# Kernel tuning notes

Measured on AMD Instinct MI355X. Metric: run time of the kernel, lower is better.

Reference implementation:

```python
import jax, jax.numpy as jnp
import numpy as np

B, IN, OUT = 8192, 512, 1024

def setup_inputs() -> dict:
    key = jax.random.key(0)
    k1, k2 = jax.random.split(key)
    return {
        "input": jax.random.normal(k1, (B, IN), dtype=jnp.float32),
        "centres": jax.random.normal(k2, (OUT, IN), dtype=jnp.float32),
        "log_sigmas": jnp.zeros((OUT,), dtype=jnp.float32),
    }

def reference(input, centres, log_sigmas):
    x_sq = jnp.sum(input * input, axis=-1, keepdims=True)          # [B, 1]
    c_sq = jnp.sum(centres * centres, axis=-1)                     # [OUT]
    cross = input @ centres.T                                      # [B, OUT] GEMM
    d2 = jnp.maximum(x_sq - 2.0 * cross + c_sq[None, :], 0.0)
    distances = jnp.sqrt(d2) / jnp.exp(log_sigmas)[None, :]        # [B, OUT]
    # gaussian basis function: phi(alpha) = exp(-alpha^2)
    return jnp.exp(-(distances * distances))
```

## Files before the change

### kernel.cpp

```cpp
#include <hip/hip_runtime.h>
#include <hip/hip_bf16.h>


#define B_ROWS 8192
#define IN_K   512
#define OUT_N  1024

#define BM 128
#define BN 128
#define BK 32
#define LDT 40

typedef __attribute__((ext_vector_type(8))) __bf16 bf16x8;
typedef __attribute__((ext_vector_type(4))) __bf16 bf16x4;
typedef __attribute__((ext_vector_type(4))) float  floatx4;

__global__ void rowsumsq_512(const float* __restrict__ x, float* __restrict__ out, int rows) {
    int gt   = blockIdx.x * blockDim.x + threadIdx.x;
    int wave = gt >> 6;
    int lane = threadIdx.x & 63;
    if (wave >= rows) return;
    const float4* r4 = reinterpret_cast<const float4*>(x + (size_t)wave * IN_K);
    float4 a = r4[lane];
    float4 b = r4[lane + 64];
    float s = a.x*a.x + a.y*a.y + a.z*a.z + a.w*a.w
            + b.x*b.x + b.y*b.y + b.z*b.z + b.w*b.w;
    #pragma unroll
    for (int off = 32; off; off >>= 1) s += __shfl_xor(s, off, 64);
    if (lane == 0) out[wave] = s;
}

__global__ __launch_bounds__(256, 2) void rbf_gemm(
    const float* __restrict__ X,
    const float* __restrict__ C,
    const float* __restrict__ LS,
    const float* __restrict__ xsq,
    const float* __restrict__ csq,
    float* __restrict__ out)
{
    __shared__ __bf16 As[BM * LDT];
    __shared__ __bf16 Bs[BN * LDT];

    const int tid  = threadIdx.x;
    const int bn   = blockIdx.x & 7;
    const int bm   = blockIdx.x >> 3;
    const int brow = bm * BM;
    const int bcol = bn * BN;
    const int w    = tid >> 6;
    const int lane = tid & 63;
    const int wr   = w >> 1;
    const int wc   = w & 1;
    const int l15  = lane & 15;
    const int l4   = lane >> 4;

    floatx4 acc[4][4];
    #pragma unroll
    for (int m = 0; m < 4; ++m)
        #pragma unroll
        for (int n = 0; n < 4; ++n)
            acc[m][n] = (floatx4){0.f, 0.f, 0.f, 0.f};

    float4 ar[4], br[4];

    auto load_tile = [&](int kt, float4* a, float4* b) {
        #pragma unroll
        for (int i = 0; i < 4; ++i) {
            int lin = i * 256 + tid;
            int r   = lin >> 3;
            int c4  = lin & 7;
            a[i] = *reinterpret_cast<const float4*>(X + (size_t)(brow + r) * IN_K + kt * BK + c4 * 4);
            b[i] = *reinterpret_cast<const float4*>(C + (size_t)(bcol + r) * IN_K + kt * BK + c4 * 4);
        }
    };
    auto store_tile = [&](const float4* a, const float4* b) {
        #pragma unroll
        for (int i = 0; i < 4; ++i) {
            int lin = i * 256 + tid;
            int r   = lin >> 3;
            int c4  = lin & 7;
            bf16x4 va = { (__bf16)a[i].x, (__bf16)a[i].y, (__bf16)a[i].z, (__bf16)a[i].w };
            bf16x4 vb = { (__bf16)b[i].x, (__bf16)b[i].y, (__bf16)b[i].z, (__bf16)b[i].w };
            *reinterpret_cast<bf16x4*>(&As[r * LDT + c4 * 4]) = va;
            *reinterpret_cast<bf16x4*>(&Bs[r * LDT + c4 * 4]) = vb;
        }
    };

    load_tile(0, ar, br);

    const int NKT = IN_K / BK;
    #pragma unroll 1
    for (int kt = 0; kt < NKT; ++kt) {
        if (kt) __syncthreads();
        store_tile(ar, br);
        __syncthreads();

        float4 ar2[4], br2[4];
        if (kt < NKT - 1) load_tile(kt + 1, ar2, br2);

        bf16x8 af[4], bfr[4];
        #pragma unroll
        for (int m = 0; m < 4; ++m)
            af[m] = *reinterpret_cast<const bf16x8*>(&As[(wr * 64 + m * 16 + l15) * LDT + l4 * 8]);
        #pragma unroll
        for (int n = 0; n < 4; ++n)
            bfr[n] = *reinterpret_cast<const bf16x8*>(&Bs[(wc * 64 + n * 16 + l15) * LDT + l4 * 8]);

        #pragma unroll
        for (int m = 0; m < 4; ++m)
            #pragma unroll
            for (int n = 0; n < 4; ++n)
                acc[m][n] = __builtin_amdgcn_mfma_f32_16x16x32_bf16(af[m], bfr[n], acc[m][n], 0, 0, 0);

        #pragma unroll
        for (int i = 0; i < 4; ++i) { ar[i] = ar2[i]; br[i] = br2[i]; }
    }

    float xs[4][4];
    #pragma unroll
    for (int m = 0; m < 4; ++m) {
        int row0 = brow + wr * 64 + m * 16 + l4 * 4;
        #pragma unroll
        for (int r = 0; r < 4; ++r) xs[m][r] = xsq[row0 + r];
    }

    #pragma unroll
    for (int n = 0; n < 4; ++n) {
        int col   = bcol + wc * 64 + n * 16 + l15;
        float cs  = csq[col];
        float inv = __expf(-2.f * LS[col]);
        #pragma unroll
        for (int m = 0; m < 4; ++m) {
            int row0 = brow + wr * 64 + m * 16 + l4 * 4;
            #pragma unroll
            for (int r = 0; r < 4; ++r) {
                float cross = acc[m][n][r];
                float d2 = fmaxf(xs[m][r] + cs - 2.f * cross, 0.f);
                out[(size_t)(row0 + r) * OUT_N + col] = __expf(-d2 * inv);
            }
        }
    }
}

extern "C" void kernel_launch(void* const* d_in, const int* in_sizes, int n_in,
                              void* d_out, int out_size, void* d_ws, size_t ws_size,
                              hipStream_t stream) {
    const float* X  = (const float*)d_in[0];
    const float* C  = (const float*)d_in[1];
    const float* LS = (const float*)d_in[2];
    float* out = (float*)d_out;
    float* xsq = (float*)d_ws;
    float* csq = xsq + B_ROWS;

    rowsumsq_512<<<B_ROWS / 4, 256, 0, stream>>>(X, xsq, B_ROWS);
    rowsumsq_512<<<OUT_N / 4, 256, 0, stream>>>(C, csq, OUT_N);
    rbf_gemm<<<(B_ROWS / BM) * (OUT_N / BN), 256, 0, stream>>>(X, C, LS, xsq, csq, out);
}
```

Measured before the change: 98.48 us.

## Pre-convert inputs to bf16 and stream tiles via direct global-to-LDS loads

A fused pre-pass now converts X and C to bf16 in workspace while also computing the row sums of squares, replacing the two separate sum-of-squares launches. The GEMM then loads bf16 tiles straight into double-buffered, XOR-swizzled LDS with global_load_lds, using BK=64 and a remapped block order for L2 locality. This removes the fp32 loads, register round trips and in-loop conversion from the GEMM. In exchange it adds an extra write and read of the bf16 copies in global memory and relies on the workspace being large enough to hold them.

```diff
diff --git a/kernel.cpp b/kernel.cpp
--- a/kernel.cpp
+++ b/kernel.cpp
@@ -5,53 +5,85 @@
 #define B_ROWS 8192
 #define IN_K   512
 #define OUT_N  1024
-
-#define BM 128
-#define BN 128
-#define BK 32
-#define LDT 40
+#define BK     64
+#define NKT    (IN_K / BK)
 
 typedef __attribute__((ext_vector_type(8))) __bf16 bf16x8;
 typedef __attribute__((ext_vector_type(4))) __bf16 bf16x4;
 typedef __attribute__((ext_vector_type(4))) float  floatx4;
 
-__global__ void rowsumsq_512(const float* __restrict__ x, float* __restrict__ out, int rows) {
-    int gt   = blockIdx.x * blockDim.x + threadIdx.x;
-    int wave = gt >> 6;
+__device__ __forceinline__ void gload_lds16(const void* g, void* l) {
+    __builtin_amdgcn_global_load_lds((const __attribute__((address_space(1))) void*)g,
+                                     (__attribute__((address_space(3))) void*)l,
+                                     16, 0, 0);
+}
+
+__global__ __launch_bounds__(256) void convert_sumsq(
+    const float* __restrict__ X, const float* __restrict__ C,
+    __bf16* __restrict__ Xbf, __bf16* __restrict__ Cbf,
+    float* __restrict__ xsq, float* __restrict__ csq)
+{
+    int wid  = (blockIdx.x * 256 + threadIdx.x) >> 6;
     int lane = threadIdx.x & 63;
-    if (wave >= rows) return;
-    const float4* r4 = reinterpret_cast<const float4*>(x + (size_t)wave * IN_K);
-    float4 a = r4[lane];
-    float4 b = r4[lane + 64];
+    const float* src; __bf16* dst; float* sq;
+    if (wid < B_ROWS) {
+        src = X + (size_t)wid * IN_K; dst = Xbf + (size_t)wid * IN_K; sq = xsq + wid;
+    } else {
+        int r = wid - B_ROWS;
+        src = C + (size_t)r * IN_K;  dst = Cbf + (size_t)r * IN_K;  sq = csq + r;
+    }
+    const float4* s4 = reinterpret_cast<const float4*>(src);
+    float4 a = s4[lane];
+    float4 b = s4[lane + 64];
+    bf16x4 va = {(__bf16)a.x, (__bf16)a.y, (__bf16)a.z, (__bf16)a.w};
+    bf16x4 vb = {(__bf16)b.x, (__bf16)b.y, (__bf16)b.z, (__bf16)b.w};
+    *reinterpret_cast<bf16x4*>(dst + lane * 4)       = va;
+    *reinterpret_cast<bf16x4*>(dst + 256 + lane * 4) = vb;
     float s = a.x*a.x + a.y*a.y + a.z*a.z + a.w*a.w
             + b.x*b.x + b.y*b.y + b.z*b.z + b.w*b.w;
     #pragma unroll
     for (int off = 32; off; off >>= 1) s += __shfl_xor(s, off, 64);
-    if (lane == 0) out[wave] = s;
+    if (lane == 0) *sq = s;
 }
 
 __global__ __launch_bounds__(256, 2) void rbf_gemm(
-    const float* __restrict__ X,
-    const float* __restrict__ C,
+    const __bf16* __restrict__ Xbf,
+    const __bf16* __restrict__ Cbf,
     const float* __restrict__ LS,
     const float* __restrict__ xsq,
     const float* __restrict__ csq,
     float* __restrict__ out)
 {
-    __shared__ __bf16 As[BM * LDT];
-    __shared__ __bf16 Bs[BN * LDT];
+    __shared__ __bf16 As[2][128 * BK];
+    __shared__ __bf16 Bs[2][128 * BK];
 
     const int tid  = threadIdx.x;
-    const int bn   = blockIdx.x & 7;
-    const int bm   = blockIdx.x >> 3;
-    const int brow = bm * BM;
-    const int bcol = bn * BN;
+    const int sid  = blockIdx.x;
+    const int bidx = (sid & 7) * 64 + (sid >> 3);
+    const int bm   = bidx >> 3;
+    const int bn   = bidx & 7;
+    const int brow = bm * 128;
+    const int bcol = bn * 128;
+    const int lane = tid & 63;
     const int w    = tid >> 6;
-    const int lane = tid & 63;
     const int wr   = w >> 1;
     const int wc   = w & 1;
     const int l15  = lane & 15;
     const int l4   = lane >> 4;
+
+    const int srow = tid >> 3;
+    const int col8 = (((tid & 7) ^ (srow & 7)) * 8);
+    const __bf16* Asrc = Xbf + (size_t)(brow + srow) * IN_K + col8;
+    const __bf16* Bsrc = Cbf + (size_t)(bcol + srow) * IN_K + col8;
+
+    auto stage = [&](int kt, int buf) {
+        #pragma unroll
+        for (int i = 0; i < 4; ++i)
+            gload_lds16(Asrc + (size_t)i * 32 * IN_K + kt * BK, &As[buf][tid * 8 + i * 2048]);
+        #pragma unroll
+        for (int i = 0; i < 4; ++i)
+            gload_lds16(Bsrc + (size_t)i * 32 * IN_K + kt * BK, &Bs[buf][tid * 8 + i * 2048]);
+    };
 
     floatx4 acc[4][4];
     #pragma unroll
@@ -60,59 +92,37 @@
         for (int n = 0; n < 4; ++n)
             acc[m][n] = (floatx4){0.f, 0.f, 0.f, 0.f};
 
-    float4 ar[4], br[4];
+    stage(0, 0);
 
-    auto load_tile = [&](int kt, float4* a, float4* b) {
-        #pragma unroll
-        for (int i = 0; i < 4; ++i) {
-            int lin = i * 256 + tid;
-            int r   = lin >> 3;
-            int c4  = lin & 7;
-            a[i] = *reinterpret_cast<const float4*>(X + (size_t)(brow + r) * IN_K + kt * BK + c4 * 4);
-            b[i] = *reinterpret_cast<const float4*>(C + (size_t)(bcol + r) * IN_K + kt * BK + c4 * 4);
-        }
-    };
-    auto store_tile = [&](const float4* a, const float4* b) {
-        #pragma unroll
-        for (int i = 0; i < 4; ++i) {
-            int lin = i * 256 + tid;
-            int r   = lin >> 3;
-            int c4  = lin & 7;
-            bf16x4 va = { (__bf16)a[i].x, (__bf16)a[i].y, (__bf16)a[i].z, (__bf16)a[i].w };
-            bf16x4 vb = { (__bf16)b[i].x, (__bf16)b[i].y, (__bf16)b[i].z, (__bf16)b[i].w };
-            *reinterpret_cast<bf16x4*>(&As[r * LDT + c4 * 4]) = va;
-            *reinterpret_cast<bf16x4*>(&Bs[r * LDT + c4 * 4]) = vb;
-        }
-    };
-
-    load_tile(0, ar, br);
-
-    const int NKT = IN_K / BK;
     #pragma unroll 1
     for (int kt = 0; kt < NKT; ++kt) {
-        if (kt) __syncthreads();
-        store_tile(ar, br);
+        const int cur = kt & 1;
         __syncthreads();
-
-        float4 ar2[4], br2[4];
-        if (kt < NKT - 1) load_tile(kt + 1, ar2, br2);
-
-        bf16x8 af[4], bfr[4];
-        #pragma unroll
-        for (int m = 0; m < 4; ++m)
-            af[m] = *reinterpret_cast<const bf16x8*>(&As[(wr * 64 + m * 16 + l15) * LDT + l4 * 8]);
-        #pragma unroll
-        for (int n = 0; n < 4; ++n)
-            bfr[n] = *reinterpret_cast<const bf16x8*>(&Bs[(wc * 64 + n * 16 + l15) * LDT + l4 * 8]);
+        if (kt < NKT - 1) stage(kt + 1, cur ^ 1);
 
         #pragma unroll
-        for (int m = 0; m < 4; ++m)
+        for (int ks = 0; ks < 2; ++ks) {
+            bf16x8 af[4], bfr[4];
             #pragma unroll
-            for (int n = 0; n < 4; ++n)
-                acc[m][n] = __builtin_amdgcn_mfma_f32_16x16x32_bf16(af[m], bfr[n], acc[m][n], 0, 0, 0);
-
-        #pragma unroll
-        for (int i = 0; i < 4; ++i) { ar[i] = ar2[i]; br[i] = br2[i]; }
+            for (int m = 0; m < 4; ++m) {
+                int r = wr * 64 + m * 16 + l15;
+                int kslot = l4 + ks * 4;
+                af[m] = *reinterpret_cast<const bf16x8*>(
+                    &As[cur][r * BK + ((kslot ^ (r & 7)) * 8)]);
+            }
+            #pragma unroll
+            for (int n = 0; n < 4; ++n) {
+                int r = wc * 64 + n * 16 + l15;
+                int kslot = l4 + ks * 4;
+                bfr[n] = *reinterpret_cast<const bf16x8*>(
+                    &Bs[cur][r * BK + ((kslot ^ (r & 7)) * 8)]);
+            }
+            #pragma unroll
+            for (int m = 0; m < 4; ++m)
+                #pragma unroll
+                for (int n = 0; n < 4; ++n)
+                    acc[m][n] = __builtin_amdgcn_mfma_f32_16x16x32_bf16(af[m], bfr[n], acc[m][n], 0, 0, 0);
+        }
     }
 
     float xs[4][4];
@@ -148,10 +158,12 @@
     const float* C  = (const float*)d_in[1];
     const float* LS = (const float*)d_in[2];
     float* out = (float*)d_out;
-    float* xsq = (float*)d_ws;
-    float* csq = xsq + B_ROWS;
 
-    rowsumsq_512<<<B_ROWS / 4, 256, 0, stream>>>(X, xsq, B_ROWS);
-    rowsumsq_512<<<OUT_N / 4, 256, 0, stream>>>(C, csq, OUT_N);
-    rbf_gemm<<<(B_ROWS / BM) * (OUT_N / BN), 256, 0, stream>>>(X, C, LS, xsq, csq, out);
+    float*  xsq = (float*)d_ws;
+    float*  csq = (float*)((char*)d_ws + 32768);
+    __bf16* Xbf = (__bf16*)((char*)d_ws + 65536);
+    __bf16* Cbf = (__bf16*)((char*)d_ws + 65536 + (size_t)B_ROWS * IN_K * 2);
+
+    convert_sumsq<<<(B_ROWS + OUT_N) / 4, 256, 0, stream>>>(X, C, Xbf, Cbf, xsq, csq);
+    rbf_gemm<<<(B_ROWS / 128) * (OUT_N / 128), 256, 0, stream>>>(Xbf, Cbf, LS, xsq, csq, out);
 }
```

Measured after the change: 88.14 us. 10.5% less time.
